# Performance work log

Hardware: AMD Instinct MI355X
Metric: run time of the kernel (lower is better)

The kernel has to match this reference:

```python
import jax, jax.numpy as jnp
import numpy as np

N = 200_000      # active voxels
INC = 64
OUTC = 96
GRID = 128
EPS = 1e-5


def _build_neighbor_maps():
    """Precompute gather/scatter index maps for the 26 off-center hypercube
    offsets (the 4th kernel dim has size 1, so offsets live in 3D)."""
    rng = np.random.default_rng(0)
    G = GRID ** 3
    lin = rng.choice(G, size=N, replace=False).astype(np.int64)
    z = lin % GRID
    y = (lin // GRID) % GRID
    x = lin // (GRID * GRID)
    lookup = np.full(G, -1, np.int64)
    lookup[lin] = np.arange(N)
    offsets = [(dx, dy, dz) for dx in (-1, 0, 1) for dy in (-1, 0, 1)
               for dz in (-1, 0, 1) if (dx, dy, dz) != (0, 0, 0)]
    pin, pout = [], []
    for dx, dy, dz in offsets:
        nx, ny, nz = x + dx, y + dy, z + dz
        valid = (nx >= 0) & (nx < GRID) & (ny >= 0) & (ny < GRID) & (nz >= 0) & (nz < GRID)
        nlin = (nx * GRID + ny) * GRID + nz
        nb = np.where(valid, lookup[np.clip(nlin, 0, G - 1)], -1)
        m = nb >= 0
        pin.append(np.arange(N)[m])
        pout.append(nb[m])
    pmax = max(len(p) for p in pin)
    in_idx = np.zeros((26, pmax), np.int64)          # pad gathers row 0 (harmless)
    out_idx = np.full((26, pmax), N, np.int64)       # pad scatters to sink row N
    for k, (pi, po) in enumerate(zip(pin, pout)):
        in_idx[k, : len(pi)] = pi
        out_idx[k, : len(po)] = po
    return in_idx, out_idx


def setup_inputs() -> dict:
    in_idx, out_idx = _build_neighbor_maps()
    key = jax.random.key(0)
    k1, k2, k3 = jax.random.split(key, 3)
    std = 1.0 / np.sqrt(INC * 27)
    feats = jax.random.normal(k1, (N, INC), jnp.float32)
    W_center = jax.random.normal(k2, (INC, OUTC), jnp.float32) * std
    W_off = jax.random.normal(k3, (26, INC, OUTC), jnp.float32) * std
    gamma = jnp.ones((OUTC,), jnp.float32)   # bn.weight init to 1.0
    beta = jnp.zeros((OUTC,), jnp.float32)   # bn.bias init to 0.0
    return {"feats": feats, "W_center": W_center, "W_off": W_off,
            "gamma": gamma, "beta": beta,
            "in_idx": jnp.asarray(in_idx), "out_idx": jnp.asarray(out_idx)}


def reference(feats, W_center, W_off, gamma, beta, in_idx, out_idx):
    # --- sparse conv-transpose: gather -> GEMM -> scatter-add ---
    out = feats @ W_center                                   # center offset: identity map, [N, outc]
    gathered = feats[in_idx]                                 # [26, P, inc]
    contrib = jnp.einsum('kpc,kcd->kpd', gathered, W_off)    # [26, P, outc]
    out = jnp.concatenate([out, jnp.zeros((1, OUTC), out.dtype)], axis=0)  # sink row
    out = out.at[out_idx.reshape(-1)].add(contrib.reshape(-1, OUTC))[:N]
    # --- BatchNorm (training-mode batch stats) + ReLU ---
    mean = out.mean(axis=0)
    var = out.var(axis=0)
    y = (out - mean) * jax.lax.rsqrt(var + EPS) * gamma + beta
    return jax.nn.relu(y)
```

## Files before the change

### kernel.cpp

```cpp
#include <hip/hip_runtime.h>


#define N_VOX   200000
#define INC     64
#define OUTC    96
#define NOFF    26
#define NBLK    782
#define EPSV    1e-5f

using bf16x8 = __attribute__((ext_vector_type(8))) short;
using f32x4  = __attribute__((ext_vector_type(4))) float;

__device__ inline unsigned short f2bf(float x) {
    union { float f; unsigned u; } v; v.f = x;
    unsigned r = (v.u + 0x7FFFu + ((v.u >> 16) & 1u)) >> 16;
    return (unsigned short)r;
}

__device__ __forceinline__ void gload_lds16(const void* g, void* l) {
    __builtin_amdgcn_global_load_lds(
        (const __attribute__((address_space(1))) void*)g,
        (__attribute__((address_space(3))) void*)l, 16, 0, 0);
}

__global__ void fill_src_kernel(const int* __restrict__ in_idx,
                                const int* __restrict__ out_idx,
                                int P, int* __restrict__ srcmap) {
    int idx = blockIdx.x * blockDim.x + threadIdx.x;
    if (idx >= NOFF * P) return;
    int dst = out_idx[idx];
    if (dst >= N_VOX) return;
    int k = idx / P;
    srcmap[(size_t)k * N_VOX + dst] = in_idx[idx];
}

__global__ void wprep_kernel(const float* __restrict__ Wc,
                             const float* __restrict__ Woff,
                             unsigned short* __restrict__ Wb) {
    int t = blockIdx.x * blockDim.x + threadIdx.x;
    if (t >= 27 * 2 * 6 * 64) return;
    int lane = t & 63;
    int g    = t >> 6;
    int ct   = g % 6;
    int s    = (g / 6) % 2;
    int m    = g / 12;
    const float* W = (m == 26) ? Wc : (Woff + (size_t)m * INC * OUTC);
    int k0 = s * 32 + (lane >> 4) * 8;
    int c  = ct * 16 + (lane & 15);
    bf16x8 v;
    #pragma unroll
    for (int e = 0; e < 8; ++e)
        v[e] = (short)f2bf(W[(size_t)(k0 + e) * OUTC + c]);
    *(bf16x8*)(Wb + (size_t)t * 8) = v;
}

__global__ void fcvt_kernel(const float* __restrict__ feats,
                            unsigned short* __restrict__ featsb) {
    int i = blockIdx.x * blockDim.x + threadIdx.x;
    if (i >= N_VOX * INC / 8) return;
    const float4* src = (const float4*)feats + (size_t)i * 2;
    float4 f0 = src[0], f1 = src[1];
    bf16x8 v;
    v[0] = (short)f2bf(f0.x); v[1] = (short)f2bf(f0.y);
    v[2] = (short)f2bf(f0.z); v[3] = (short)f2bf(f0.w);
    v[4] = (short)f2bf(f1.x); v[5] = (short)f2bf(f1.y);
    v[6] = (short)f2bf(f1.z); v[7] = (short)f2bf(f1.w);
    *(bf16x8*)(featsb + (size_t)i * 8) = v;
}

__global__ __launch_bounds__(256, 2)
void conv_mfma_kernel(const unsigned short* __restrict__ featsb,
                      const unsigned short* __restrict__ Wb,
                      const int* __restrict__ srcmap,
                      float* __restrict__ out,
                      float* __restrict__ pstats) {
    __shared__ __align__(16) unsigned short Wlds[2][6144];

    const int t     = threadIdx.x;
    const int wid   = t >> 6;
    const int lane  = t & 63;
    const int blk   = blockIdx.x;
    const int rbase = blk * 256 + wid * 64;
    const int row16 = lane & 15;
    const int kgrp  = lane >> 4;

    f32x4  acc[4][6] = {};
    bf16x8 aC[4][2] = {}, aN[4][2] = {};

    #pragma unroll
    for (int i = 0; i < 3; ++i)
        gload_lds16(Wb + (size_t)26 * 6144 + (size_t)(t + 256 * i) * 8,
                    &Wlds[0][(t + 256 * i) * 8]);

    int sm_next = -1;
    {
        int row = rbase + lane;
        if (row < N_VOX) sm_next = srcmap[row];
    }
    bool has_cur = false;
    #pragma unroll
    for (int rt = 0; rt < 4; ++rt) {
        int src = rbase + rt * 16 + row16;
        if (src < N_VOX) {
            const unsigned short* fr = featsb + (size_t)src * INC + kgrp * 8;
            aC[rt][0] = *(const bf16x8*)fr;
            aC[rt][1] = *(const bf16x8*)(fr + 32);
            has_cur = true;
        }
    }
    has_cur = __ballot(has_cur) != 0ull;
    __syncthreads();

    for (int idx = 0; idx < 27; ++idx) {
        const int buf = idx & 1;

        int sm_next2 = -1;
        if (idx <= 24) {
            int row = rbase + lane;
            if (row < N_VOX) sm_next2 = srcmap[(size_t)(idx + 1) * N_VOX + row];
        }

        bool has_next = false;
        if (idx <= 25) {
            bool any = false;
            #pragma unroll
            for (int rt = 0; rt < 4; ++rt) {
                int src = __shfl(sm_next, rt * 16 + row16);
                bf16x8 g0 = {}, g1 = {};
                if (src >= 0) {
                    const unsigned short* fr = featsb + (size_t)src * INC + kgrp * 8;
                    g0 = *(const bf16x8*)fr;
                    g1 = *(const bf16x8*)(fr + 32);
                    any = true;
                }
                aN[rt][0] = g0; aN[rt][1] = g1;
            }
            has_next = __ballot(any) != 0ull;
            #pragma unroll
            for (int i = 0; i < 3; ++i)
                gload_lds16(Wb + (size_t)idx * 6144 + (size_t)(t + 256 * i) * 8,
                            &Wlds[buf ^ 1][(t + 256 * i) * 8]);
        }

        if (has_cur) {
            const unsigned short* WL = Wlds[buf];
            #pragma unroll
            for (int ct = 0; ct < 6; ++ct) {
                bf16x8 b0 = *(const bf16x8*)&WL[(size_t)ct * 512 + lane * 8];
                bf16x8 b1 = *(const bf16x8*)&WL[(size_t)(6 + ct) * 512 + lane * 8];
                #pragma unroll
                for (int rt = 0; rt < 4; ++rt) {
                    acc[rt][ct] = __builtin_amdgcn_mfma_f32_16x16x32_bf16(aC[rt][0], b0, acc[rt][ct], 0, 0, 0);
                    acc[rt][ct] = __builtin_amdgcn_mfma_f32_16x16x32_bf16(aC[rt][1], b1, acc[rt][ct], 0, 0, 0);
                }
            }
        }
        __syncthreads();

        #pragma unroll
        for (int rt = 0; rt < 4; ++rt) { aC[rt][0] = aN[rt][0]; aC[rt][1] = aN[rt][1]; }
        sm_next = sm_next2;
        has_cur = has_next;
    }

    float s6[6], q6[6];
    #pragma unroll
    for (int ct = 0; ct < 6; ++ct) {
        float s = 0.f, q = 0.f;
        #pragma unroll
        for (int rt = 0; rt < 4; ++rt) {
            f32x4 a = acc[rt][ct];
            s += a[0] + a[1] + a[2] + a[3];
            q += a[0]*a[0] + a[1]*a[1] + a[2]*a[2] + a[3]*a[3];
        }
        s += __shfl_xor(s, 16); q += __shfl_xor(q, 16);
        s += __shfl_xor(s, 32); q += __shfl_xor(q, 32);
        s6[ct] = s; q6[ct] = q;
    }
    float* sred = (float*)Wlds;
    if (lane < 16) {
        #pragma unroll
        for (int ct = 0; ct < 6; ++ct) {
            sred[wid * 96 + ct * 16 + lane]       = s6[ct];
            sred[384 + wid * 96 + ct * 16 + lane] = q6[ct];
        }
    }
    __syncthreads();
    if (t < 96) {
        float s = sred[t] + sred[96 + t] + sred[192 + t] + sred[288 + t];
        pstats[(size_t)t * NBLK + blk] = s;
    } else if (t < 192) {
        int c = t - 96;
        float q = sred[384 + c] + sred[480 + c] + sred[576 + c] + sred[672 + c];
        pstats[(size_t)(96 + c) * NBLK + blk] = q;
    }

    #pragma unroll
    for (int rt = 0; rt < 4; ++rt) {
        #pragma unroll
        for (int ct = 0; ct < 6; ++ct) {
            #pragma unroll
            for (int j = 0; j < 4; ++j) {
                int row = rbase + rt * 16 + kgrp * 4 + j;
                if (row < N_VOX)
                    out[(size_t)row * OUTC + ct * 16 + row16] = acc[rt][ct][j];
            }
        }
    }
}

__global__ void stats_reduce_kernel(const float* __restrict__ pstats,
                                    const float* __restrict__ gamma,
                                    const float* __restrict__ beta,
                                    float* __restrict__ scsh) {
    int c = blockIdx.x;
    int t = threadIdx.x;
    float s = 0.f, q = 0.f;
    for (int i = t; i < NBLK; i += 256) {
        s += pstats[(size_t)c * NBLK + i];
        q += pstats[(size_t)(96 + c) * NBLK + i];
    }
    #pragma unroll
    for (int d = 1; d < 64; d <<= 1) {
        s += __shfl_xor(s, d);
        q += __shfl_xor(q, d);
    }
    __shared__ float rs[4], rq[4];
    if ((t & 63) == 0) { rs[t >> 6] = s; rq[t >> 6] = q; }
    __syncthreads();
    if (t == 0) {
        s = rs[0] + rs[1] + rs[2] + rs[3];
        q = rq[0] + rq[1] + rq[2] + rq[3];
        float inv_n = 1.0f / (float)N_VOX;
        float mean = s * inv_n;
        float var  = q * inv_n - mean * mean;
        float sc   = gamma[c] * rsqrtf(var + EPSV);
        scsh[c]      = sc;
        scsh[96 + c] = beta[c] - mean * sc;
    }
}

__global__ void apply_bn_kernel(float* __restrict__ out,
                                const float* __restrict__ scsh) {
    __shared__ float sc[OUTC], sh[OUTC];
    int t = threadIdx.x;
    if (t < OUTC) { sc[t] = scsh[t]; sh[t] = scsh[96 + t]; }
    __syncthreads();
    const int total4 = N_VOX * OUTC / 4;
    for (int i = blockIdx.x * blockDim.x + t; i < total4; i += gridDim.x * blockDim.x) {
        float4 v = ((float4*)out)[i];
        int c = (i * 4) % OUTC;
        v.x = fmaxf(fmaf(v.x, sc[c    ], sh[c    ]), 0.f);
        v.y = fmaxf(fmaf(v.y, sc[c + 1], sh[c + 1]), 0.f);
        v.z = fmaxf(fmaf(v.z, sc[c + 2], sh[c + 2]), 0.f);
        v.w = fmaxf(fmaf(v.w, sc[c + 3], sh[c + 3]), 0.f);
        ((float4*)out)[i] = v;
    }
}

extern "C" void kernel_launch(void* const* d_in, const int* in_sizes, int n_in,
                              void* d_out, int out_size, void* d_ws, size_t ws_size,
                              hipStream_t stream) {
    const float* feats   = (const float*)d_in[0];
    const float* Wc      = (const float*)d_in[1];
    const float* Woff    = (const float*)d_in[2];
    const float* gamma   = (const float*)d_in[3];
    const float* beta    = (const float*)d_in[4];
    const int*   in_idx  = (const int*)d_in[5];
    const int*   out_idx = (const int*)d_in[6];
    const int P = in_sizes[5] / NOFF;

    char* w = (char*)d_ws;
    int* srcmap = (int*)w;                   w += (size_t)NOFF * N_VOX * 4;
    unsigned short* Wb = (unsigned short*)w; w += (size_t)27 * 6144 * 2;
    float* pstats = (float*)w;               w += (size_t)192 * NBLK * 4;
    float* scsh = (float*)w;                 w += 256 * 4;
    unsigned short* featsb = (unsigned short*)w;

    hipMemsetAsync(srcmap, 0xFF, (size_t)NOFF * N_VOX * 4, stream);
    fill_src_kernel<<<(NOFF * P + 255) / 256, 256, 0, stream>>>(in_idx, out_idx, P, srcmap);
    wprep_kernel<<<(27 * 2 * 6 * 64 + 255) / 256, 256, 0, stream>>>(Wc, Woff, Wb);
    fcvt_kernel<<<(N_VOX * INC / 8 + 255) / 256, 256, 0, stream>>>(feats, featsb);

    float* out = (float*)d_out;
    conv_mfma_kernel<<<NBLK, 256, 0, stream>>>(featsb, Wb, srcmap, out, pstats);
    stats_reduce_kernel<<<96, 256, 0, stream>>>(pstats, gamma, beta, scsh);
    apply_bn_kernel<<<2048, 256, 0, stream>>>(out, scsh);
}
```

Baseline: 130.3 us.

## Pipeline neighbor gathers with padded srcmap, zero sink row, and bf16 staging

Pads srcmap to NPAD rows and adds a zero sink feature row, so gathers run branch-free and each lane loads its own srcmap entry instead of shuffling one. The srcmap prefetch is moved one stage ahead, and the full __syncthreads is replaced by a partial vmcnt wait plus s_barrier. MFMAs are skipped per 16-row tile when no lane in the tile has a neighbor. When the workspace is large enough, the conv output is staged as bf16 and the BN pass expands it to fp32, halving the intermediate write and read. This adds extra rounding error before BatchNorm, and the hand-written vmcnt count is fragile.

```diff
diff --git a/kernel.cpp b/kernel.cpp
--- a/kernel.cpp
+++ b/kernel.cpp
@@ -6,9 +6,11 @@
 #define OUTC    96
 #define NOFF    26
 #define NBLK    782
+#define NPAD    200192
 #define EPSV    1e-5f
 
 using bf16x8 = __attribute__((ext_vector_type(8))) short;
+using u16x8  = __attribute__((ext_vector_type(8))) unsigned short;
 using f32x4  = __attribute__((ext_vector_type(4))) float;
 
 __device__ inline unsigned short f2bf(float x) {
@@ -31,7 +33,7 @@
     int dst = out_idx[idx];
     if (dst >= N_VOX) return;
     int k = idx / P;
-    srcmap[(size_t)k * N_VOX + dst] = in_idx[idx];
+    srcmap[(size_t)k * NPAD + dst] = in_idx[idx];
 }
 
 __global__ void wprep_kernel(const float* __restrict__ Wc,
@@ -68,11 +70,13 @@
     *(bf16x8*)(featsb + (size_t)i * 8) = v;
 }
 
+template<int STAGE_BF16>
 __global__ __launch_bounds__(256, 2)
 void conv_mfma_kernel(const unsigned short* __restrict__ featsb,
                       const unsigned short* __restrict__ Wb,
                       const int* __restrict__ srcmap,
-                      float* __restrict__ out,
+                      float* __restrict__ outf,
+                      unsigned short* __restrict__ stg,
                       float* __restrict__ pstats) {
     __shared__ __align__(16) unsigned short Wlds[2][6144];
 
@@ -85,64 +89,63 @@
     const int kgrp  = lane >> 4;
 
     f32x4  acc[4][6] = {};
-    bf16x8 aC[4][2] = {}, aN[4][2] = {};
+    bf16x8 aC[4][2], aN[4][2];
+    int smC[4], smN[4];
+    int hasC, hasN;
 
     #pragma unroll
     for (int i = 0; i < 3; ++i)
         gload_lds16(Wb + (size_t)26 * 6144 + (size_t)(t + 256 * i) * 8,
                     &Wlds[0][(t + 256 * i) * 8]);
-
-    int sm_next = -1;
-    {
-        int row = rbase + lane;
-        if (row < N_VOX) sm_next = srcmap[row];
-    }
-    bool has_cur = false;
+    #pragma unroll
+    for (int rt = 0; rt < 4; ++rt)
+        smC[rt] = srcmap[rbase + rt * 16 + row16];
     #pragma unroll
     for (int rt = 0; rt < 4; ++rt) {
-        int src = rbase + rt * 16 + row16;
-        if (src < N_VOX) {
-            const unsigned short* fr = featsb + (size_t)src * INC + kgrp * 8;
-            aC[rt][0] = *(const bf16x8*)fr;
-            aC[rt][1] = *(const bf16x8*)(fr + 32);
-            has_cur = true;
-        }
-    }
-    has_cur = __ballot(has_cur) != 0ull;
-    __syncthreads();
-
+        int row = rbase + rt * 16 + row16;
+        int src = row < N_VOX ? row : N_VOX;
+        const unsigned short* fr = featsb + (size_t)src * INC + kgrp * 8;
+        aC[rt][0] = *(const bf16x8*)fr;
+        aC[rt][1] = *(const bf16x8*)(fr + 32);
+    }
+    hasC = 0xF;
+    asm volatile("s_waitcnt vmcnt(0)" ::: "memory");
+    __builtin_amdgcn_s_barrier();
+
+    #pragma unroll 2
     for (int idx = 0; idx < 27; ++idx) {
         const int buf = idx & 1;
 
-        int sm_next2 = -1;
-        if (idx <= 24) {
-            int row = rbase + lane;
-            if (row < N_VOX) sm_next2 = srcmap[(size_t)(idx + 1) * N_VOX + row];
-        }
-
-        bool has_next = false;
-        if (idx <= 25) {
-            bool any = false;
+        if (idx < 26) {
+            const unsigned short* wsrc = Wb + (size_t)idx * 6144;
+            #pragma unroll
+            for (int i = 0; i < 3; ++i)
+                gload_lds16(wsrc + (size_t)(t + 256 * i) * 8,
+                            &Wlds[buf ^ 1][(t + 256 * i) * 8]);
+        }
+        asm volatile("" ::: "memory");
+
+        {
+            int off = idx + 1; if (off > 25) off = 25;
+            #pragma unroll
+            for (int rt = 0; rt < 4; ++rt)
+                smN[rt] = srcmap[(size_t)off * NPAD + rbase + rt * 16 + row16];
+        }
+        {
+            int h = 0;
             #pragma unroll
             for (int rt = 0; rt < 4; ++rt) {
-                int src = __shfl(sm_next, rt * 16 + row16);
-                bf16x8 g0 = {}, g1 = {};
-                if (src >= 0) {
-                    const unsigned short* fr = featsb + (size_t)src * INC + kgrp * 8;
-                    g0 = *(const bf16x8*)fr;
-                    g1 = *(const bf16x8*)(fr + 32);
-                    any = true;
-                }
-                aN[rt][0] = g0; aN[rt][1] = g1;
+                if (__ballot(smC[rt] >= 0)) h |= (1 << rt);
+                int src = smC[rt] >= 0 ? smC[rt] : N_VOX;
+                const unsigned short* fr = featsb + (size_t)src * INC + kgrp * 8;
+                aN[rt][0] = *(const bf16x8*)fr;
+                aN[rt][1] = *(const bf16x8*)(fr + 32);
             }
-            has_next = __ballot(any) != 0ull;
-            #pragma unroll
-            for (int i = 0; i < 3; ++i)
-                gload_lds16(Wb + (size_t)idx * 6144 + (size_t)(t + 256 * i) * 8,
-                            &Wlds[buf ^ 1][(t + 256 * i) * 8]);
-        }
-
-        if (has_cur) {
+            hasN = __builtin_amdgcn_readfirstlane(h);
+        }
+        asm volatile("" ::: "memory");
+
+        {
             const unsigned short* WL = Wlds[buf];
             #pragma unroll
             for (int ct = 0; ct < 6; ++ct) {
@@ -150,18 +153,24 @@
                 bf16x8 b1 = *(const bf16x8*)&WL[(size_t)(6 + ct) * 512 + lane * 8];
                 #pragma unroll
                 for (int rt = 0; rt < 4; ++rt) {
-                    acc[rt][ct] = __builtin_amdgcn_mfma_f32_16x16x32_bf16(aC[rt][0], b0, acc[rt][ct], 0, 0, 0);
-                    acc[rt][ct] = __builtin_amdgcn_mfma_f32_16x16x32_bf16(aC[rt][1], b1, acc[rt][ct], 0, 0, 0);
+                    if (hasC & (1 << rt)) {
+                        acc[rt][ct] = __builtin_amdgcn_mfma_f32_16x16x32_bf16(aC[rt][0], b0, acc[rt][ct], 0, 0, 0);
+                        acc[rt][ct] = __builtin_amdgcn_mfma_f32_16x16x32_bf16(aC[rt][1], b1, acc[rt][ct], 0, 0, 0);
+                    }
                 }
             }
         }
-        __syncthreads();
-
-        #pragma unroll
-        for (int rt = 0; rt < 4; ++rt) { aC[rt][0] = aN[rt][0]; aC[rt][1] = aN[rt][1]; }
-        sm_next = sm_next2;
-        has_cur = has_next;
-    }
+
+        asm volatile("s_waitcnt vmcnt(12)" ::: "memory");
+        __builtin_amdgcn_s_barrier();
+
+        #pragma unroll
+        for (int rt = 0; rt < 4; ++rt) {
+            aC[rt][0] = aN[rt][0]; aC[rt][1] = aN[rt][1]; smC[rt] = smN[rt];
+        }
+        hasC = hasN;
+    }
+    __syncthreads();
 
     float s6[6], q6[6];
     #pragma unroll
@@ -202,8 +211,12 @@
             #pragma unroll
             for (int j = 0; j < 4; ++j) {
                 int row = rbase + rt * 16 + kgrp * 4 + j;
-                if (row < N_VOX)
-                    out[(size_t)row * OUTC + ct * 16 + row16] = acc[rt][ct][j];
+                if (row < N_VOX) {
+                    if (STAGE_BF16)
+                        stg[(size_t)row * OUTC + ct * 16 + row16] = f2bf(acc[rt][ct][j]);
+                    else
+                        outf[(size_t)row * OUTC + ct * 16 + row16] = acc[rt][ct][j];
+                }
             }
         }
     }
@@ -240,8 +253,31 @@
     }
 }
 
-__global__ void apply_bn_kernel(float* __restrict__ out,
-                                const float* __restrict__ scsh) {
+__global__ void apply_bn_bf16_kernel(const unsigned short* __restrict__ stg,
+                                     float* __restrict__ out,
+                                     const float* __restrict__ scsh) {
+    __shared__ float sc[OUTC], sh[OUTC];
+    int t = threadIdx.x;
+    if (t < OUTC) { sc[t] = scsh[t]; sh[t] = scsh[96 + t]; }
+    __syncthreads();
+    const int total8 = N_VOX * OUTC / 8;
+    for (int i = blockIdx.x * blockDim.x + t; i < total8; i += gridDim.x * blockDim.x) {
+        u16x8 v = *(const u16x8*)(stg + (size_t)i * 8);
+        int c = (i % 12) * 8;
+        float o[8];
+        #pragma unroll
+        for (int j = 0; j < 8; ++j) {
+            union { unsigned u; float f; } w; w.u = (unsigned)v[j] << 16;
+            o[j] = fmaxf(fmaf(w.f, sc[c + j], sh[c + j]), 0.f);
+        }
+        float4* dst = (float4*)(out + (size_t)i * 8);
+        dst[0] = make_float4(o[0], o[1], o[2], o[3]);
+        dst[1] = make_float4(o[4], o[5], o[6], o[7]);
+    }
+}
+
+__global__ void apply_bn_fp32_kernel(float* __restrict__ out,
+                                     const float* __restrict__ scsh) {
     __shared__ float sc[OUTC], sh[OUTC];
     int t = threadIdx.x;
     if (t < OUTC) { sc[t] = scsh[t]; sh[t] = scsh[96 + t]; }
@@ -271,19 +307,30 @@
     const int P = in_sizes[5] / NOFF;
 
     char* w = (char*)d_ws;
-    int* srcmap = (int*)w;                   w += (size_t)NOFF * N_VOX * 4;
+    int* srcmap = (int*)w;                   w += (size_t)NOFF * NPAD * 4;
     unsigned short* Wb = (unsigned short*)w; w += (size_t)27 * 6144 * 2;
     float* pstats = (float*)w;               w += (size_t)192 * NBLK * 4;
     float* scsh = (float*)w;                 w += 256 * 4;
     unsigned short* featsb = (unsigned short*)w;
-
-    hipMemsetAsync(srcmap, 0xFF, (size_t)NOFF * N_VOX * 4, stream);
+    w += (size_t)(N_VOX + 1) * INC * 2;
+    unsigned short* stg = (unsigned short*)w;
+    size_t need_stg = (size_t)(w - (char*)d_ws) + (size_t)N_VOX * OUTC * 2;
+    bool use_stg = (ws_size >= need_stg);
+
+    hipMemsetAsync(srcmap, 0xFF, (size_t)NOFF * NPAD * 4, stream);
+    hipMemsetAsync(featsb + (size_t)N_VOX * INC, 0, INC * 2, stream);
     fill_src_kernel<<<(NOFF * P + 255) / 256, 256, 0, stream>>>(in_idx, out_idx, P, srcmap);
     wprep_kernel<<<(27 * 2 * 6 * 64 + 255) / 256, 256, 0, stream>>>(Wc, Woff, Wb);
     fcvt_kernel<<<(N_VOX * INC / 8 + 255) / 256, 256, 0, stream>>>(feats, featsb);
 
     float* out = (float*)d_out;
-    conv_mfma_kernel<<<NBLK, 256, 0, stream>>>(featsb, Wb, srcmap, out, pstats);
-    stats_reduce_kernel<<<96, 256, 0, stream>>>(pstats, gamma, beta, scsh);
-    apply_bn_kernel<<<2048, 256, 0, stream>>>(out, scsh);
-}
+    if (use_stg) {
+        conv_mfma_kernel<1><<<NBLK, 256, 0, stream>>>(featsb, Wb, srcmap, out, stg, pstats);
+        stats_reduce_kernel<<<96, 256, 0, stream>>>(pstats, gamma, beta, scsh);
+        apply_bn_bf16_kernel<<<2048, 256, 0, stream>>>(stg, out, scsh);
+    } else {
+        conv_mfma_kernel<0><<<NBLK, 256, 0, stream>>>(featsb, Wb, srcmap, out, stg, pstats);
+        stats_reduce_kernel<<<96, 256, 0, stream>>>(pstats, gamma, beta, scsh);
+        apply_bn_fp32_kernel<<<2048, 256, 0, stream>>>(out, scsh);
+    }
+}
```

Result: slower. 142.7 us (+9.5%).
